# Optimization experiments

Hardware: AMD Instinct MI355X
Metric: run time of the kernel (lower is better)

The kernel has to match this reference:

```python
import jax, jax.numpy as jnp
import numpy as np
from jax import lax


def conv3x3(x, w):
    # x: (B,C,H,W), w: (O,I,3,3); stride 1, padding 1, no bias
    return lax.conv_general_dilated(x, w, (1, 1), 'SAME',
                                    dimension_numbers=('NCHW', 'OIHW', 'NCHW'))


def group_norm(x, w, b, groups=32, eps=1e-5):
    B, C, H, W = x.shape
    xg = x.reshape(B, groups, C // groups, H, W)
    mu = xg.mean(axis=(2, 3, 4), keepdims=True)
    var = xg.var(axis=(2, 3, 4), keepdims=True)
    xg = (xg - mu) * lax.rsqrt(var + eps)
    return xg.reshape(B, C, H, W) * w[None, :, None, None] + b[None, :, None, None]


def to_patches(x, p1, p2):
    # 'b c (h p1) (w p2) -> (b h w) c (p1 p2)'
    B, C, H, W = x.shape
    h, w = H // p1, W // p2
    x = x.reshape(B, C, h, p1, w, p2).transpose(0, 2, 4, 1, 3, 5)
    return x.reshape(B * h * w, C, p1 * p2)


def from_patches(x, B, h, w, p1, p2):
    # '(b h w) c (p1 p2) -> b c (h p1) (w p2)'
    C = x.shape[1]
    x = x.reshape(B, h, w, C, p1, p2).transpose(0, 3, 1, 4, 2, 5)
    return x.reshape(B, C, h * p1, w * p2)


def setup_inputs() -> dict:
    key = jax.random.key(0)
    ks = jax.random.split(key, 5)
    B, C, H, W = 8, 256, 128, 128
    inter = 256
    s = 0.05  # keep conv outputs in a sane range
    return {
        'x_low': jax.random.normal(ks[0], (B, C, H, W), jnp.float32),
        'x_high': jax.random.normal(ks[1], (B, C, H, W), jnp.float32),
        'w_q': jax.random.normal(ks[2], (inter, C, 3, 3), jnp.float32) * s,
        'gq_w': jnp.ones((inter,), jnp.float32),
        'gq_b': jnp.zeros((inter,), jnp.float32),
        'w_k': jax.random.normal(ks[3], (inter, C, 3, 3), jnp.float32) * s,
        'gk_w': jnp.ones((inter,), jnp.float32),
        'gk_b': jnp.zeros((inter,), jnp.float32),
        'w_o': jax.random.normal(ks[4], (C, inter, 3, 3), jnp.float32) * s,
        'go_w': jnp.ones((C,), jnp.float32),
        'go_b': jnp.zeros((C,), jnp.float32),
        'p1': 8,
        'p2': 8,
    }


def reference(x_low, x_high, w_q, gq_w, gq_b, w_k, gk_w, gk_b, w_o, go_w, go_b, p1, p2):
    B, C, H, W = x_low.shape
    inter = w_q.shape[0]
    h, w = H // p1, W // p2
    # q, k: (B*h*w, inter, T) with T = p1*p2
    q = to_patches(group_norm(conv3x3(x_low, w_q), gq_w, gq_b), p1, p2)
    k = to_patches(group_norm(conv3x3(x_high, w_k), gk_w, gk_b), p1, p2)
    q = q.transpose(0, 2, 1)                                  # (N, T, inter)
    attn = jnp.matmul(q, k) / jnp.sqrt(jnp.float32(inter))    # (N, T, T)
    attn = jax.nn.softmax(attn, axis=-1)
    out = jnp.matmul(attn, k.transpose(0, 2, 1))              # (N, T, inter)
    out = from_patches(out.transpose(0, 2, 1), B, h, w, p1, p2)
    return group_norm(conv3x3(out + x_low, w_o), go_w, go_b)
```

## Files before the change

kernel.cpp:

```cpp
#include <hip/hip_runtime.h>

using u16 = unsigned short;
using u32 = unsigned int;

typedef short bfrag8 __attribute__((ext_vector_type(8)));
typedef float f32x4  __attribute__((ext_vector_type(4)));

__device__ __forceinline__ void unpack8(const int4 v, float f[8]) {
  u32 a = (u32)v.x, b = (u32)v.y, c = (u32)v.z, d = (u32)v.w;
  f[0] = __uint_as_float(a << 16);
  f[1] = __uint_as_float(a & 0xffff0000u);
  f[2] = __uint_as_float(b << 16);
  f[3] = __uint_as_float(b & 0xffff0000u);
  f[4] = __uint_as_float(c << 16);
  f[5] = __uint_as_float(c & 0xffff0000u);
  f[6] = __uint_as_float(d << 16);
  f[7] = __uint_as_float(d & 0xffff0000u);
}

__device__ __forceinline__ u16 f2bf(float f) {
  u32 u = __float_as_uint(f);
  u32 r = u + 0x7fffu + ((u >> 16) & 1u);
  return (u16)(r >> 16);
}

__device__ __forceinline__ void gload_lds16(const void* g, void* l) {
  __builtin_amdgcn_global_load_lds(
      (const __attribute__((address_space(1))) void*)g,
      (__attribute__((address_space(3))) void*)l, 16, 0, 0);
}

__global__ __launch_bounds__(256) void wprep(
    const float* __restrict__ wq, const float* __restrict__ wk, const float* __restrict__ wo,
    u16* __restrict__ dq, u16* __restrict__ dk, u16* __restrict__ dwo)
{
  const float* s = (blockIdx.y == 0) ? wq : (blockIdx.y == 1) ? wk : wo;
  u16* d = (blockIdx.y == 0) ? dq : (blockIdx.y == 1) ? dk : dwo;
  int id = blockIdx.x * 256 + threadIdx.x;
  int e = id * 4;
  int tap = e >> 16;
  int rem = e & 65535;
  int oc = rem >> 8, ic = rem & 255;
  u16 o[4];
#pragma unroll
  for (int j = 0; j < 4; ++j)
    o[j] = f2bf(s[((size_t)oc * 256 + ic + j) * 9 + tap]);
  *reinterpret_cast<uint2*>(d + e) = *reinterpret_cast<uint2*>(o);
}

__global__ __launch_bounds__(256) void xpose(
    const float* __restrict__ xa, const float* __restrict__ xb,
    u16* __restrict__ oa, u16* __restrict__ ob)
{
  const int row = blockIdx.x, b = blockIdx.y;
  const float* src = blockIdx.z ? xb : xa;
  u16* dst = blockIdx.z ? ob : oa;
  const int t = threadIdx.x;
  const int px4 = (t >> 3) * 4;
  const int c8 = (t & 7) * 8;
#pragma unroll
  for (int p = 0; p < 4; ++p) {
    int c0 = p * 64 + c8;
    float4 v[8];
#pragma unroll
    for (int j = 0; j < 8; ++j)
      v[j] = *reinterpret_cast<const float4*>(src + ((size_t)b * 256 + c0 + j) * 16384 + row * 128 + px4);
#pragma unroll
    for (int e = 0; e < 4; ++e) {
      u16 o[8];
      o[0] = f2bf(e==0?v[0].x:e==1?v[0].y:e==2?v[0].z:v[0].w);
      o[1] = f2bf(e==0?v[1].x:e==1?v[1].y:e==2?v[1].z:v[1].w);
      o[2] = f2bf(e==0?v[2].x:e==1?v[2].y:e==2?v[2].z:v[2].w);
      o[3] = f2bf(e==0?v[3].x:e==1?v[3].y:e==2?v[3].z:v[3].w);
      o[4] = f2bf(e==0?v[4].x:e==1?v[4].y:e==2?v[4].z:v[4].w);
      o[5] = f2bf(e==0?v[5].x:e==1?v[5].y:e==2?v[5].z:v[5].w);
      o[6] = f2bf(e==0?v[6].x:e==1?v[6].y:e==2?v[6].z:v[6].w);
      o[7] = f2bf(e==0?v[7].x:e==1?v[7].y:e==2?v[7].z:v[7].w);
      *reinterpret_cast<int4*>(dst + (((size_t)b * 128 + row) * 128 + px4 + e) * 256 + c0) =
          *reinterpret_cast<int4*>(o);
    }
  }
}

__global__ __launch_bounds__(256, 3) void conv_mfma(
    const u16* __restrict__ X, const u16* __restrict__ W2, u16* __restrict__ Y,
    float* __restrict__ part, u16* __restrict__ kTout)
{
  __shared__ __attribute__((aligned(16))) char csm[49920];

  const int t = threadIdx.x;
  const int l = t & 63;
  const int wv = t >> 6;
  const int id = blockIdx.x;
  const int u = (id & 7) * 256 + (id >> 3);
  const int bb = u >> 8;
  const int y0 = (u >> 1) & 127;
  const int ocblk = u & 1;
  const int oc0 = ocblk * 128;
  const int och = wv >> 1, pxh = wv & 1;
  const int lc = l & 15, lq = l >> 4;
  const int sa = (lc >> 1) & 3;

  f32x4 acc[4][4];
#pragma unroll
  for (int m = 0; m < 4; ++m)
#pragma unroll
    for (int n = 0; n < 4; ++n) acc[m][n] = (f32x4){0.f, 0.f, 0.f, 0.f};

  const size_t xplane = (size_t)bb * (128 * 128 * 256);

  {
    int4 z = {0, 0, 0, 0};
    if (t < 24) {
      int q = t & 3, sel = (t >> 2) & 1, kh = t >> 3;
      int cidx = sel ? 129 : 0;
      *reinterpret_cast<int4*>(csm + ((kh * 132 + cidx) * 4 + q) * 16) = z;
    }
    if (y0 == 0)
      for (int s = t; s < 528; s += 256) *reinterpret_cast<int4*>(csm + s * 16) = z;
    if (y0 == 127)
      for (int s = t; s < 528; s += 256) *reinterpret_cast<int4*>(csm + 16896 + s * 16) = z;
  }

  auto stageA = [&](int tap, int buf, int ic0) {
#pragma unroll
    for (int i = 0; i < 2; ++i) {
      int idx = t + i * 256;
      int oc = idx >> 2, q = idx & 3;
      int qs = q ^ ((oc >> 1) & 3);
      const u16* src = W2 + (((size_t)(tap * 256 + oc0 + oc)) << 8) + ic0 + qs * 8;
      gload_lds16(src, csm + 25344 + buf * 8192 + (i * 256 + (t & ~63)) * 16);
    }
  };
  auto stageB = [&](int ic0) {
#pragma unroll
    for (int i = 0; i < 6; ++i) {
      int idx = t + i * 256;
      int kh = idx >> 9;
      int row = y0 - 1 + kh;
      if (row >= 0 && row < 128) {
        int px = (idx & 511) >> 2, q = idx & 3;
        int qs = q ^ (((px + 1) >> 1) & 3);
        const u16* src = X + xplane + (((size_t)(row * 128 + px)) << 8) + ic0 + qs * 8;
        gload_lds16(src, csm + 64 + kh * 256 + (i * 256 + (t & ~63)) * 16);
      }
    }
  };

  bfrag8 af0[4], xf0[4], af1[4], xf1[4];

#define READF(TAP, AF, XF)                                                    \
  {                                                                           \
    const int kh_ = (TAP) / 3, kw_ = (TAP) % 3, buf_ = (TAP) % 3;             \
    const int sb_ = ((lc + kw_) >> 1) & 3;                                    \
    _Pragma("unroll")                                                         \
    for (int m = 0; m < 4; ++m)                                               \
      AF[m] = *reinterpret_cast<const bfrag8*>(csm + 25344 + buf_ * 8192 +    \
                  ((och * 64 + m * 16 + lc) * 4 + (lq ^ sa)) * 16);           \
    _Pragma("unroll")                                                         \
    for (int n = 0; n < 4; ++n) {                                             \
      int S_ = pxh * 64 + n * 16 + lc + kw_;                                  \
      XF[n] = *reinterpret_cast<const bfrag8*>(csm + kh_ * 8448 + S_ * 64 +   \
                  (lq ^ sb_) * 16);                                           \
    }                                                                         \
  }

#define DOMFMA(AF, XF)                                                        \
  {                                                                           \
    _Pragma("unroll")                                                         \
    for (int m = 0; m < 4; ++m)                                               \
      _Pragma("unroll")                                                       \
      for (int n = 0; n < 4; ++n)                                             \
        acc[m][n] = __builtin_amdgcn_mfma_f32_16x16x32_bf16(AF[m], XF[n],     \
                                                            acc[m][n], 0, 0, 0); \
  }

  stageB(0);
  stageA(0, 0, 0);
  stageA(1, 1, 0);
  __syncthreads();

  for (int chunk = 0; chunk < 8; ++chunk) {
    const int ic0 = chunk * 32;
    READF(0, af0, xf0);
#pragma unroll
    for (int tap = 0; tap < 9; ++tap) {
      asm volatile("s_waitcnt lgkmcnt(0)" ::: "memory");
      __builtin_amdgcn_sched_barrier(0);
      if (tap <= 6) stageA(tap + 2, (tap + 2) % 3, ic0);
      if (tap <= 6) {
        asm volatile("s_waitcnt vmcnt(2)" ::: "memory");
      } else if (tap == 7) {
        asm volatile("s_waitcnt vmcnt(0)" ::: "memory");
      }
      __builtin_amdgcn_sched_barrier(0);
      __builtin_amdgcn_s_barrier();
      __builtin_amdgcn_sched_barrier(0);

      if (tap < 8) {
        if (tap & 1) { READF(tap + 1, af0, xf0); }
        else         { READF(tap + 1, af1, xf1); }
      }
      __builtin_amdgcn_s_setprio(1);
      if (tap & 1) { DOMFMA(af1, xf1); }
      else         { DOMFMA(af0, xf0); }
      __builtin_amdgcn_s_setprio(0);
    }
    if (chunk < 7) {
      stageA(0, 0, ic0 + 32);
      stageA(1, 1, ic0 + 32);
      stageB(ic0 + 32);
      __syncthreads();
    }
  }
#undef READF
#undef DOMFMA

  u16* Ost = (u16*)csm;
  float* sst = (float*)(csm + 34816);
  const int chb = och * 64 + lq * 4;
  const int pxb = pxh * 64 + lc;
  __syncthreads();
#pragma unroll
  for (int m = 0; m < 4; ++m)
#pragma unroll
    for (int n = 0; n < 4; ++n) {
      u32 lo = (u32)f2bf(acc[m][n][0]) | ((u32)f2bf(acc[m][n][1]) << 16);
      u32 hi = (u32)f2bf(acc[m][n][2]) | ((u32)f2bf(acc[m][n][3]) << 16);
      uint2 pk = {lo, hi};
      *reinterpret_cast<uint2*>(&Ost[(pxb + n * 16) * 136 + chb + m * 16]) = pk;
    }
#pragma unroll
  for (int m = 0; m < 4; ++m)
#pragma unroll
    for (int r = 0; r < 4; ++r) {
      float s  = acc[m][0][r] + acc[m][1][r] + acc[m][2][r] + acc[m][3][r];
      float ss = acc[m][0][r] * acc[m][0][r] + acc[m][1][r] * acc[m][1][r] +
                 acc[m][2][r] * acc[m][2][r] + acc[m][3][r] * acc[m][3][r];
#pragma unroll
      for (int off = 1; off < 16; off <<= 1) {
        s  += __shfl_xor(s, off);
        ss += __shfl_xor(ss, off);
      }
      if (lc == 0) {
        int c = och * 64 + m * 16 + lq * 4 + r;
        sst[pxh * 256 + c]       = s;
        sst[pxh * 256 + 128 + c] = ss;
      }
    }
  __syncthreads();

  if (t < 128) {
    float s  = sst[t]       + sst[256 + t];
    float ss = sst[128 + t] + sst[384 + t];
    size_t pb = (((size_t)bb * 128 + y0) * 256 + oc0 + t) * 2;
    part[pb]     = s;
    part[pb + 1] = ss;
  }
#pragma unroll
  for (int s8 = 0; s8 < 8; ++s8) {
    int pix = s8 * 16 + (t >> 4);
    int sub = t & 15;
    int4 v = *reinterpret_cast<const int4*>(&Ost[pix * 136 + sub * 8]);
    *reinterpret_cast<int4*>(Y + xplane + (((size_t)(y0 * 128 + pix)) << 8) + oc0 + sub * 8) = v;
  }

  if (kTout) {
    const size_t outbase = ((size_t)(bb * 16 + (y0 >> 3)) * 8 + (y0 & 7)) * 32768;
    const int half = t >> 7;
    const int cl = t & 127;
#pragma unroll
    for (int i = 0; i < 8; ++i) {
      int pw = i * 2 + half;
      u16 o[8];
#pragma unroll
      for (int j = 0; j < 8; ++j) o[j] = Ost[(pw * 8 + j) * 136 + cl];
      *reinterpret_cast<int4*>(kTout + outbase + (size_t)(pw * 256 + oc0 + cl) * 8) =
          *reinterpret_cast<int4*>(o);
    }
  }
}

__global__ __launch_bounds__(256) void gnstat2b(const float* __restrict__ part, float* __restrict__ stat)
{
  const int b = blockIdx.x, t = threadIdx.x;
  float s = 0.f, ss = 0.f;
  for (int row = 0; row < 128; ++row) {
    size_t pb = (((size_t)b * 128 + row) * 256 + t) * 2;
    s  += part[pb];
    ss += part[pb + 1];
  }
  __shared__ float Ls[256], Lss[256];
  Ls[t] = s; Lss[t] = ss;
  __syncthreads();
  if (t < 32) {
    float S = 0.f, SS = 0.f;
#pragma unroll
    for (int j = 0; j < 8; ++j) { S += Ls[t * 8 + j]; SS += Lss[t * 8 + j]; }
    float mean = S * (1.f / 131072.f);
    float var = SS * (1.f / 131072.f) - mean * mean;
    stat[b * 32 + t] = mean;
    stat[256 + b * 32 + t] = rsqrtf(var + 1e-5f);
  }
}

#define OST 272
__global__ __launch_bounds__(256, 3) void attn_mfma(
    const u16* __restrict__ yq, const u16* __restrict__ yk,
    const u16* __restrict__ kT, const u16* __restrict__ xl,
    const float* __restrict__ statq, const float* __restrict__ statk,
    const float* __restrict__ gqw, const float* __restrict__ gqb,
    const float* __restrict__ gkw, const float* __restrict__ gkb,
    u16* __restrict__ resid)
{
  __shared__ __attribute__((aligned(16))) u16 smem[64 * OST + 4 * 16 * 72];
  u16* Ost = smem;
  u16* Pls = smem + 64 * OST;

  const int n = blockIdx.x;
  const int b = n >> 8, ph = (n >> 4) & 15, pw = n & 15;
  const int t = threadIdx.x, l = t & 63, w = t >> 6;
  const int lc = l & 15, lg = l >> 4;

  auto tokaddr = [&](int tok) -> size_t {
    return (((size_t)(b * 128 + ph * 8 + (tok >> 3))) * 128 + pw * 8 + (tok & 7)) * 256;
  };

  const size_t qa = tokaddr(16 * w + lc) + lg * 8;
  bfrag8 aF[8];
#pragma unroll
  for (int ks = 0; ks < 8; ++ks) {
    int c0 = lg * 8 + ks * 32;
    int g = ks * 4 + lg;
    float meanq = statq[b * 32 + g], rstdq = statq[256 + b * 32 + g];
    float rstdk = statk[256 + b * 32 + g];
    int4 v = *reinterpret_cast<const int4*>(yq + qa + ks * 32);
    float f[8]; unpack8(v, f);
    float4 w0 = *reinterpret_cast<const float4*>(gqw + c0);
    float4 w1 = *reinterpret_cast<const float4*>(gqw + c0 + 4);
    float4 b0 = *reinterpret_cast<const float4*>(gqb + c0);
    float4 b1 = *reinterpret_cast<const float4*>(gqb + c0 + 4);
    float4 k0 = *reinterpret_cast<const float4*>(gkw + c0);
    float4 k1 = *reinterpret_cast<const float4*>(gkw + c0 + 4);
    float ww[8] = {w0.x, w0.y, w0.z, w0.w, w1.x, w1.y, w1.z, w1.w};
    float bb[8] = {b0.x, b0.y, b0.z, b0.w, b1.x, b1.y, b1.z, b1.w};
    float kk[8] = {k0.x, k0.y, k0.z, k0.w, k1.x, k1.y, k1.z, k1.w};
    u16 o[8];
#pragma unroll
    for (int j = 0; j < 8; ++j) {
      float Aq = rstdq * ww[j];
      float Bq = bb[j] - meanq * Aq;
      float Ak = rstdk * kk[j];
      o[j] = f2bf((f[j] * Aq + Bq) * Ak);
    }
    aF[ks] = *reinterpret_cast<bfrag8*>(o);
  }

  f32x4 sacc[4];
#pragma unroll
  for (int nt = 0; nt < 4; ++nt) sacc[nt] = (f32x4){0.f, 0.f, 0.f, 0.f};

#pragma unroll
  for (int nt = 0; nt < 4; ++nt) {
    const size_t ka = tokaddr(nt * 16 + lc) + lg * 8;
    bfrag8 bF[8];
#pragma unroll
    for (int ks = 0; ks < 8; ++ks)
      bF[ks] = *reinterpret_cast<const bfrag8*>(yk + ka + ks * 32);
#pragma unroll
    for (int ks = 0; ks < 8; ++ks)
      sacc[nt] = __builtin_amdgcn_mfma_f32_16x16x32_bf16(aF[ks], bF[ks], sacc[nt], 0, 0, 0);
  }

  u16* Pw = Pls + w * (16 * 72);
#pragma unroll
  for (int r = 0; r < 4; ++r) {
    float m0 = fmaxf(fmaxf(sacc[0][r], sacc[1][r]), fmaxf(sacc[2][r], sacc[3][r]));
    m0 = fmaxf(m0, __shfl_xor(m0, 1));
    m0 = fmaxf(m0, __shfl_xor(m0, 2));
    m0 = fmaxf(m0, __shfl_xor(m0, 4));
    m0 = fmaxf(m0, __shfl_xor(m0, 8));
    float p0 = __expf((sacc[0][r] - m0) * 0.0625f);
    float p1 = __expf((sacc[1][r] - m0) * 0.0625f);
    float p2 = __expf((sacc[2][r] - m0) * 0.0625f);
    float p3 = __expf((sacc[3][r] - m0) * 0.0625f);
    float s0 = p0 + p1 + p2 + p3;
    s0 += __shfl_xor(s0, 1);
    s0 += __shfl_xor(s0, 2);
    s0 += __shfl_xor(s0, 4);
    s0 += __shfl_xor(s0, 8);
    float inv = 1.f / s0;
    int prow = (lg * 4 + r) * 72;
    Pw[prow + 0 * 16 + lc] = f2bf(p0 * inv);
    Pw[prow + 1 * 16 + lc] = f2bf(p1 * inv);
    Pw[prow + 2 * 16 + lc] = f2bf(p2 * inv);
    Pw[prow + 3 * 16 + lc] = f2bf(p3 * inv);
  }

  bfrag8 pA[2];
#pragma unroll
  for (int js = 0; js < 2; ++js)
    pA[js] = *reinterpret_cast<const bfrag8*>(Pw + lc * 72 + js * 32 + lg * 8);

  f32x4 pacc[16];
#pragma unroll
  for (int ct = 0; ct < 16; ++ct) pacc[ct] = (f32x4){0.f, 0.f, 0.f, 0.f};

#pragma unroll
  for (int ct = 0; ct < 16; ++ct) {
    bfrag8 vB[2];
#pragma unroll
    for (int js = 0; js < 2; ++js)
      vB[js] = *reinterpret_cast<const bfrag8*>(
          kT + ((size_t)((b * 16 + ph) * 8 + js * 4 + lg)) * 32768 +
          (size_t)(pw * 256 + ct * 16 + lc) * 8);
#pragma unroll
    for (int js = 0; js < 2; ++js)
      pacc[ct] = __builtin_amdgcn_mfma_f32_16x16x32_bf16(pA[js], vB[js], pacc[ct], 0, 0, 0);
  }

#pragma unroll
  for (int ct = 0; ct < 16; ++ct) {
    int c = ct * 16 + lc;
    int g = c >> 3;
    float mean = statk[b * 32 + g], rstd = statk[256 + b * 32 + g];
    float A = rstd * gkw[c];
    float Bv = gkb[c] - mean * A;
#pragma unroll
    for (int r = 0; r < 4; ++r)
      Ost[(16 * w + lg * 4 + r) * OST + ct * 16 + lc] = f2bf(fmaf(pacc[ct][r], A, Bv));
  }
  __syncthreads();

#pragma unroll
  for (int s = 0; s < 8; ++s) {
    int px_ = t >> 5;
    int c16 = t & 31;
    size_t g = (((size_t)b * 128 + ph * 8 + s) * 128 + pw * 8 + px_) * 256 + c16 * 8;
    int4 o = *reinterpret_cast<const int4*>(&Ost[(s * 8 + px_) * OST + c16 * 8]);
    int4 r = *reinterpret_cast<const int4*>(xl + g);
    float fo[8], fr[8]; unpack8(o, fo); unpack8(r, fr);
    u16 pk[8];
#pragma unroll
    for (int j = 0; j < 8; ++j) pk[j] = f2bf(fo[j] + fr[j]);
    *reinterpret_cast<int4*>(resid + g) = *reinterpret_cast<int4*>(pk);
  }
}

__global__ __launch_bounds__(256) void gnapply_t(
    const u16* __restrict__ Y, const float* __restrict__ stat,
    const float* __restrict__ gw, const float* __restrict__ gb,
    float* __restrict__ out)
{
  const int row = blockIdx.x, b = blockIdx.y;
  const int t = threadIdx.x;
  const int px4 = (t & 31) * 4;
  const int c8 = (t >> 5) * 8;
#pragma unroll
  for (int p = 0; p < 4; ++p) {
    int c0 = p * 64 + c8;
    int g = c0 >> 3;
    float mean = stat[b * 32 + g], rstd = stat[256 + b * 32 + g];
    float A[8], Bv[8];
#pragma unroll
    for (int j = 0; j < 8; ++j) {
      A[j] = rstd * gw[c0 + j];
      Bv[j] = gb[c0 + j] - mean * A[j];
    }
    float vals[4][8];
#pragma unroll
    for (int e = 0; e < 4; ++e) {
      int4 v = *reinterpret_cast<const int4*>(Y + (((size_t)b * 128 + row) * 128 + px4 + e) * 256 + c0);
      float f[8]; unpack8(v, f);
#pragma unroll
      for (int j = 0; j < 8; ++j) vals[e][j] = fmaf(f[j], A[j], Bv[j]);
    }
#pragma unroll
    for (int j = 0; j < 8; ++j) {
      float4 o = {vals[0][j], vals[1][j], vals[2][j], vals[3][j]};
      *reinterpret_cast<float4*>(out + ((size_t)b * 256 + c0 + j) * 16384 + row * 128 + px4) = o;
    }
  }
}

extern "C" void kernel_launch(void* const* d_in, const int* in_sizes, int n_in,
                              void* d_out, int out_size, void* d_ws, size_t ws_size,
                              hipStream_t stream)
{
  const float* x_low  = (const float*)d_in[0];
  const float* x_high = (const float*)d_in[1];
  const float* w_q    = (const float*)d_in[2];
  const float* gq_w   = (const float*)d_in[3];
  const float* gq_b   = (const float*)d_in[4];
  const float* w_k    = (const float*)d_in[5];
  const float* gk_w   = (const float*)d_in[6];
  const float* gk_b   = (const float*)d_in[7];
  const float* w_o    = (const float*)d_in[8];
  const float* go_w   = (const float*)d_in[9];
  const float* go_b   = (const float*)d_in[10];
  float* out = (float*)d_out;

  char* ws = (char*)d_ws;
  const size_t slot = 67108864;
  u16* xl  = (u16*)(ws + 0 * slot);
  u16* xh  = (u16*)(ws + 1 * slot);
  u16* yq  = (u16*)(ws + 2 * slot);
  u16* yk  = (u16*)(ws + 3 * slot);
  u16* kT  = (u16*)(ws + 4 * slot);
  u16* W2q = (u16*)(ws + 5 * slot);
  u16* W2k = W2q + 589824;
  u16* W2o = W2k + 589824;
  float* partq = (float*)(ws + 5 * slot + 3 * 1179648);
  float* partk = partq + 524288;
  float* parto = partk + 524288;
  float* statq = parto + 524288;
  float* statk = statq + 512;
  float* stato = statk + 512;

  wprep<<<dim3(576, 3), 256, 0, stream>>>(w_q, w_k, w_o, W2q, W2k, W2o);
  xpose<<<dim3(128, 8, 2), 256, 0, stream>>>(x_low, x_high, xl, xh);
  conv_mfma<<<2048, 256, 0, stream>>>(xl, W2q, yq, partq, nullptr);
  conv_mfma<<<2048, 256, 0, stream>>>(xh, W2k, yk, partk, kT);
  gnstat2b<<<8, 256, 0, stream>>>(partq, statq);
  gnstat2b<<<8, 256, 0, stream>>>(partk, statk);
  attn_mfma<<<2048, 256, 0, stream>>>(yq, yk, kT, xl, statq, statk,
                                      gq_w, gq_b, gk_w, gk_b, xh);
  conv_mfma<<<2048, 256, 0, stream>>>(xh, W2o, xl, parto, nullptr);
  gnstat2b<<<8, 256, 0, stream>>>(parto, stato);
  gnapply_t<<<dim3(128, 8), 256, 0, stream>>>(xl, stato, go_w, go_b, out);
}
```

Before: 686.0 us.

## Load conv weights directly to registers and double-buffer input rows in LDS

The conv kernel stops staging weight tiles through LDS and instead loads each tap's weight fragments straight from global memory into registers, one tap ahead. The input-row staging moves to two LDS buffers, so the next channel chunk is prefetched during the current chunk. This removes the per-tap block barriers, leaving one barrier per chunk. The cost is more global loads per wave (weights are no longer shared across waves through LDS), tuned vmcnt wait counts that depend on boundary rows, and slightly more LDS.

```diff
diff --git a/kernel.cpp b/kernel.cpp
--- a/kernel.cpp
+++ b/kernel.cpp
@@ -86,7 +86,7 @@
     const u16* __restrict__ X, const u16* __restrict__ W2, u16* __restrict__ Y,
     float* __restrict__ part, u16* __restrict__ kTout)
 {
-  __shared__ __attribute__((aligned(16))) char csm[49920];
+  __shared__ __attribute__((aligned(16))) char csm[50688];
 
   const int t = threadIdx.x;
   const int l = t & 63;
@@ -99,7 +99,7 @@
   const int oc0 = ocblk * 128;
   const int och = wv >> 1, pxh = wv & 1;
   const int lc = l & 15, lq = l >> 4;
-  const int sa = (lc >> 1) & 3;
+  const bool full = (y0 != 0) && (y0 != 127);
 
   f32x4 acc[4][4];
 #pragma unroll
@@ -111,28 +111,25 @@
 
   {
     int4 z = {0, 0, 0, 0};
-    if (t < 24) {
-      int q = t & 3, sel = (t >> 2) & 1, kh = t >> 3;
+    if (t < 48) {
+      int bufp = t / 24, r = t % 24;
+      int q = r & 3, sel = (r >> 2) & 1, kh = r >> 3;
       int cidx = sel ? 129 : 0;
-      *reinterpret_cast<int4*>(csm + ((kh * 132 + cidx) * 4 + q) * 16) = z;
+      *reinterpret_cast<int4*>(csm + bufp * 25344 + ((kh * 132 + cidx) * 4 + q) * 16) = z;
     }
     if (y0 == 0)
-      for (int s = t; s < 528; s += 256) *reinterpret_cast<int4*>(csm + s * 16) = z;
+      for (int s = t; s < 1056; s += 256) {
+        int bufp = (s >= 528), s2 = s - bufp * 528;
+        *reinterpret_cast<int4*>(csm + bufp * 25344 + s2 * 16) = z;
+      }
     if (y0 == 127)
-      for (int s = t; s < 528; s += 256) *reinterpret_cast<int4*>(csm + 16896 + s * 16) = z;
-  }
-
-  auto stageA = [&](int tap, int buf, int ic0) {
-#pragma unroll
-    for (int i = 0; i < 2; ++i) {
-      int idx = t + i * 256;
-      int oc = idx >> 2, q = idx & 3;
-      int qs = q ^ ((oc >> 1) & 3);
-      const u16* src = W2 + (((size_t)(tap * 256 + oc0 + oc)) << 8) + ic0 + qs * 8;
-      gload_lds16(src, csm + 25344 + buf * 8192 + (i * 256 + (t & ~63)) * 16);
-    }
-  };
-  auto stageB = [&](int ic0) {
+      for (int s = t; s < 1056; s += 256) {
+        int bufp = (s >= 528), s2 = s - bufp * 528;
+        *reinterpret_cast<int4*>(csm + bufp * 25344 + 16896 + s2 * 16) = z;
+      }
+  }
+
+  auto stageB = [&](int ic0, int bufp) {
 #pragma unroll
     for (int i = 0; i < 6; ++i) {
       int idx = t + i * 256;
@@ -142,78 +139,83 @@
         int px = (idx & 511) >> 2, q = idx & 3;
         int qs = q ^ (((px + 1) >> 1) & 3);
         const u16* src = X + xplane + (((size_t)(row * 128 + px)) << 8) + ic0 + qs * 8;
-        gload_lds16(src, csm + 64 + kh * 256 + (i * 256 + (t & ~63)) * 16);
+        gload_lds16(src, csm + bufp * 25344 + 64 + kh * 256 + (i * 256 + (t & ~63)) * 16);
       }
     }
   };
 
-  bfrag8 af0[4], xf0[4], af1[4], xf1[4];
-
-#define READF(TAP, AF, XF)                                                    \
-  {                                                                           \
-    const int kh_ = (TAP) / 3, kw_ = (TAP) % 3, buf_ = (TAP) % 3;             \
+  bfrag8 aC[4], aN[4], xC[4], xN[4];
+
+#define LOADA(TAP, IC0, AR)                                                   \
+  { _Pragma("unroll")                                                         \
+    for (int m = 0; m < 4; ++m)                                               \
+      AR[m] = *reinterpret_cast<const bfrag8*>(                               \
+          W2 + (((size_t)((TAP) * 256 + oc0 + och * 64 + m * 16 + lc)) << 8)  \
+             + (IC0) + lq * 8); }
+
+#define READX(TAP, BUFP, XR)                                                  \
+  { const int kh_ = (TAP) / 3, kw_ = (TAP) % 3;                               \
     const int sb_ = ((lc + kw_) >> 1) & 3;                                    \
-    _Pragma("unroll")                                                         \
-    for (int m = 0; m < 4; ++m)                                               \
-      AF[m] = *reinterpret_cast<const bfrag8*>(csm + 25344 + buf_ * 8192 +    \
-                  ((och * 64 + m * 16 + lc) * 4 + (lq ^ sa)) * 16);           \
     _Pragma("unroll")                                                         \
     for (int n = 0; n < 4; ++n) {                                             \
       int S_ = pxh * 64 + n * 16 + lc + kw_;                                  \
-      XF[n] = *reinterpret_cast<const bfrag8*>(csm + kh_ * 8448 + S_ * 64 +   \
-                  (lq ^ sb_) * 16);                                           \
-    }                                                                         \
-  }
+      XR[n] = *reinterpret_cast<const bfrag8*>(csm + (BUFP) * 25344 +         \
+                  kh_ * 8448 + S_ * 64 + (lq ^ sb_) * 16); } }
 
 #define DOMFMA(AF, XF)                                                        \
-  {                                                                           \
-    _Pragma("unroll")                                                         \
+  { _Pragma("unroll")                                                         \
     for (int m = 0; m < 4; ++m)                                               \
       _Pragma("unroll")                                                       \
       for (int n = 0; n < 4; ++n)                                             \
         acc[m][n] = __builtin_amdgcn_mfma_f32_16x16x32_bf16(AF[m], XF[n],     \
-                                                            acc[m][n], 0, 0, 0); \
-  }
-
-  stageB(0);
-  stageA(0, 0, 0);
-  stageA(1, 1, 0);
+                                                            acc[m][n], 0, 0, 0); }
+
+  stageB(0, 0);
   __syncthreads();
 
-  for (int chunk = 0; chunk < 8; ++chunk) {
-    const int ic0 = chunk * 32;
-    READF(0, af0, xf0);
+  for (int c = 0; c < 8; ++c) {
+    const int ic0 = c * 32;
+    const int bufp = c & 1;
+    LOADA(0, ic0, aC);
+    asm volatile("s_waitcnt vmcnt(0)" ::: "memory");
+    __builtin_amdgcn_sched_barrier(0);
+    READX(0, bufp, xC);
+    asm volatile("s_waitcnt lgkmcnt(0)" ::: "memory");
+    __builtin_amdgcn_sched_barrier(0);
 #pragma unroll
     for (int tap = 0; tap < 9; ++tap) {
+      if (tap < 8) {
+        if (tap & 1) { LOADA(tap + 1, ic0, aC); }
+        else         { LOADA(tap + 1, ic0, aN); }
+      }
+      if (tap == 1 && c < 7) stageB(ic0 + 32, bufp ^ 1);
+      if (tap == 0) {
+        asm volatile("s_waitcnt vmcnt(4)" ::: "memory");
+      } else if (tap == 8) {
+        asm volatile("s_waitcnt vmcnt(0)" ::: "memory");
+      } else if (c < 7) {
+        if (full) { asm volatile("s_waitcnt vmcnt(10)" ::: "memory"); }
+        else      { asm volatile("s_waitcnt vmcnt(8)"  ::: "memory"); }
+      } else {
+        asm volatile("s_waitcnt vmcnt(4)" ::: "memory");
+      }
       asm volatile("s_waitcnt lgkmcnt(0)" ::: "memory");
       __builtin_amdgcn_sched_barrier(0);
-      if (tap <= 6) stageA(tap + 2, (tap + 2) % 3, ic0);
-      if (tap <= 6) {
-        asm volatile("s_waitcnt vmcnt(2)" ::: "memory");
-      } else if (tap == 7) {
-        asm volatile("s_waitcnt vmcnt(0)" ::: "memory");
-      }
-      __builtin_amdgcn_sched_barrier(0);
-      __builtin_amdgcn_s_barrier();
-      __builtin_amdgcn_sched_barrier(0);
-
       if (tap < 8) {
-        if (tap & 1) { READF(tap + 1, af0, xf0); }
-        else         { READF(tap + 1, af1, xf1); }
+        if (tap & 1) { READX(tap + 1, bufp, xC); }
+        else         { READX(tap + 1, bufp, xN); }
       }
       __builtin_amdgcn_s_setprio(1);
-      if (tap & 1) { DOMFMA(af1, xf1); }
-      else         { DOMFMA(af0, xf0); }
+      if (tap & 1) { DOMFMA(aN, xN); }
+      else         { DOMFMA(aC, xC); }
       __builtin_amdgcn_s_setprio(0);
     }
-    if (chunk < 7) {
-      stageA(0, 0, ic0 + 32);
-      stageA(1, 1, ic0 + 32);
-      stageB(ic0 + 32);
-      __syncthreads();
-    }
-  }
-#undef READF
+    __builtin_amdgcn_sched_barrier(0);
+    __builtin_amdgcn_s_barrier();
+    __builtin_amdgcn_sched_barrier(0);
+  }
+#undef LOADA
+#undef READX
 #undef DOMFMA
 
   u16* Ost = (u16*)csm;
```

After: 1.136 ms. 65.5% more time.
